# Optimization experiments

Measured on AMD Instinct MI355X. Metric: run time of the kernel, lower is better.

## Reference

```python
import jax, jax.numpy as jnp
import numpy as np

N = 50000        # nodes
E = 800000       # edges (avg degree 16)
G = 64           # graphs in batch
F_IN = 9
OUT = 10


def setup_inputs() -> dict:
    key = jax.random.key(0)
    ks = jax.random.split(key, 20)
    def w(k, fi, fo):
        return jax.random.normal(k, (fi, fo), dtype=jnp.float32) * (1.0 / np.sqrt(fi))
    inp = {
        "x": jax.random.normal(ks[0], (N, F_IN), dtype=jnp.float32),
        "edge_index": jax.random.randint(ks[1], (2, E), 0, N, dtype=jnp.int64),
        "batch": jnp.sort(jax.random.randint(ks[2], (N,), 0, G, dtype=jnp.int64)),
        # GCNConv weights (PyG: x @ W then normalized scatter-add, + bias)
        "W1": w(ks[3], F_IN, 128), "b1": jnp.zeros((128,), jnp.float32),
        "W2": w(ks[4], 128, 256),  "b2": jnp.zeros((256,), jnp.float32),
        "W3": w(ks[5], 256, 256),  "b3": jnp.zeros((256,), jnp.float32),
        "W4": w(ks[6], 256, 256),  "b4": jnp.zeros((256,), jnp.float32),
        # dense head
        "Wl2": w(ks[7], 256, 128), "bl2": jnp.zeros((128,), jnp.float32),
        "Wl3": w(ks[8], 128, 128), "bl3": jnp.zeros((128,), jnp.float32),
        "Wl":  w(ks[9], 128, OUT), "bl":  jnp.zeros((OUT,), jnp.float32),
    }
    return inp


def reference(x, edge_index, batch, W1, b1, W2, b2, W3, b3, W4, b4,
              Wl2, bl2, Wl3, bl3, Wl, bl):
    # GCNConv with self-loops and symmetric deg^{-1/2} normalization
    loops = jnp.arange(N, dtype=edge_index.dtype)
    src = jnp.concatenate([edge_index[0], loops])   # [E+N]
    dst = jnp.concatenate([edge_index[1], loops])
    deg = jax.ops.segment_sum(jnp.ones_like(src, dtype=x.dtype), dst, num_segments=N)
    dinv = jax.lax.rsqrt(deg)                        # deg >= 1 due to self-loops
    norm = (dinv[src] * dinv[dst])[:, None]          # [E+N, 1]

    def conv(h, W, b):
        msg = (h @ W)[src] * norm                    # gather + normalize
        return jax.ops.segment_sum(msg, dst, num_segments=N) + b

    h = jax.nn.relu(conv(x, W1, b1))
    h = jax.nn.relu(conv(h, W2, b2))
    h = jax.nn.relu(conv(h, W3, b3))
    h = conv(h, W4, b4)                              # no relu before pool
    g = jax.ops.segment_max(h, batch, num_segments=G)  # global_max_pool -> [G, 256]
    g = jax.nn.relu(g @ Wl2 + bl2)
    g = jax.nn.relu(g @ Wl3 + bl3)
    out = g @ Wl + bl                                # [G, OUT]
    return jnp.squeeze(out)
```

## Files before the change

### kernel.cpp

```cpp
#include <hip/hip_runtime.h>
#include <float.h>

#define NN 50000
#define NE 800000
#define NG 64
#define CAP 64
#define EPT 16

typedef __attribute__((ext_vector_type(8))) _Float16 f16x8;
typedef __attribute__((ext_vector_type(4))) float f32x4;
typedef __attribute__((ext_vector_type(4))) _Float16 half4;
typedef unsigned int u32;
typedef unsigned short u16;

__device__ __forceinline__ unsigned f2mono(float f) {
  unsigned b = __float_as_uint(f);
  return (b & 0x80000000u) ? ~b : (b | 0x80000000u);
}
__device__ __forceinline__ float mono2f(unsigned u) {
  unsigned b = (u & 0x80000000u) ? (u & 0x7fffffffu) : ~u;
  return __uint_as_float(b);
}
__device__ __forceinline__ void gl_lds16(const void* g, void* l) {
  __builtin_amdgcn_global_load_lds((const __attribute__((address_space(1))) u32*)g,
                                   (__attribute__((address_space(3))) u32*)l, 16, 0, 0);
}

__global__ __launch_bounds__(256) void k_count(const int* __restrict__ src,
                                               const int* __restrict__ dst,
                                               int* __restrict__ cnt,
                                               u16* __restrict__ col) {
  int s = blockIdx.x & 7;
  int base = (blockIdx.x >> 3) * (256 * EPT) + threadIdx.x;
#pragma unroll
  for (int r = 0; r < EPT; ++r) {
    int e = base + r * 256;
    if (e >= NE) break;
    int d = dst[e];
    if ((d & 7) != s) continue;
    if ((unsigned)d >= NN) continue;
    int sv = src[e];
    if ((unsigned)sv >= NN) continue;
    int pos = atomicAdd(&cnt[d], 1);
    if (pos < CAP) col[d * CAP + pos] = (u16)sv;
  }
}

__global__ void k_dinv(const int* __restrict__ cnt, float* __restrict__ dinv,
                       const float* __restrict__ x, float* __restrict__ xs,
                       unsigned* __restrict__ g) {
  int v = blockIdx.x * blockDim.x + threadIdx.x;
  if (v >= NN) return;
  if (v < NG * 256) g[v] = 0u;
  float d = rsqrtf((float)cnt[v] + 1.0f);
  dinv[v] = d;
#pragma unroll
  for (int i = 0; i < 9; ++i) xs[v * 9 + i] = x[v * 9 + i] * d;
}

__device__ __forceinline__ void splitw1(const float* W, _Float16* Wh, _Float16* Wl,
                                        int i, int K, int Nc) {
  int k = i / Nc, n = i - k * Nc;
  float w = W[i];
  _Float16 h = (_Float16)w;
  _Float16 l = (_Float16)(w - (float)h);
  Wh[(size_t)n * K + k] = h;
  Wl[(size_t)n * K + k] = l;
}
__global__ void k_splitw3(const float* __restrict__ W2, const float* __restrict__ W3,
                          const float* __restrict__ W4,
                          _Float16* __restrict__ W2h, _Float16* __restrict__ W2l,
                          _Float16* __restrict__ W3h, _Float16* __restrict__ W3l,
                          _Float16* __restrict__ W4h, _Float16* __restrict__ W4l) {
  int i = blockIdx.x * 256 + threadIdx.x;
  const int n2 = 128 * 256, n3 = 256 * 256;
  if (i < n2) splitw1(W2, W2h, W2l, i, 128, 256);
  else if (i < n2 + n3) splitw1(W3, W3h, W3l, i - n2, 256, 256);
  else if (i < n2 + 2 * n3) splitw1(W4, W4h, W4l, i - n2 - n3, 256, 256);
}

__global__ __launch_bounds__(256) void k_l1(const float* __restrict__ xs,
                                            const float* __restrict__ W,
                                            const float* __restrict__ bias,
                                            const float* __restrict__ dinv,
                                            const int* __restrict__ cnt,
                                            const u16* __restrict__ col,
                                            _Float16* __restrict__ out) {
  __shared__ float sW[9 * 128];
  __shared__ float sb[128];
  __shared__ float sX[16][12];
  int t = threadIdx.x;
  if (t < 128) sb[t] = bias[t];
  for (int i = t; i < 9 * 128; i += 256) sW[i] = W[i];
  int g = t >> 4, l = t & 15;
  int v = blockIdx.x * 16 + g;
  int c = cnt[v]; if (c > CAP) c = CAP;
  const u16* cl = col + (size_t)v * CAP;
  float acc = (l < 9) ? xs[v * 9 + l] : 0.0f;
  int j = 0;
  for (; j + 4 <= c; j += 4) {
    ushort4 u = *(const ushort4*)(cl + j);
    float a0 = (l < 9) ? xs[(int)u.x * 9 + l] : 0.f;
    float a1 = (l < 9) ? xs[(int)u.y * 9 + l] : 0.f;
    float a2 = (l < 9) ? xs[(int)u.z * 9 + l] : 0.f;
    float a3 = (l < 9) ? xs[(int)u.w * 9 + l] : 0.f;
    acc += (a0 + a1) + (a2 + a3);
  }
  for (; j < c; ++j) {
    int u = cl[j];
    if (l < 9) acc += xs[u * 9 + l];
  }
  if (l < 9) sX[g][l] = acc * dinv[v];
  __syncthreads();
  int cc = t & 127;
  int g0 = (t >> 7) * 8;
#pragma unroll
  for (int rr = 0; rr < 8; ++rr) {
    int gi = g0 + rr;
    int r = blockIdx.x * 16 + gi;
    float a = sb[cc];
#pragma unroll
    for (int i = 0; i < 9; ++i) a += sX[gi][i] * sW[i * 128 + cc];
    out[(size_t)r * 128 + cc] = (_Float16)(fmaxf(a, 0.0f) * dinv[r]);
  }
}

__global__ __launch_bounds__(256) void k_aggs(const half4* __restrict__ h,
                                              half4* __restrict__ out,
                                              const int* __restrict__ cnt,
                                              const u16* __restrict__ col,
                                              const float* __restrict__ dinv,
                                              int rowU, int slog) {
  int bid = blockIdx.x;
  int s = bid & ((1 << slog) - 1);
  int chunk = bid >> slog;
  int g = threadIdx.x >> 4;
  int l = threadIdx.x & 15;
  int v = chunk * 16 + g;
  if (v >= NN) return;
  int so = s * 16 + l;
  int c = cnt[v]; if (c > CAP) c = CAP;
  const u16* cl = col + (size_t)v * CAP;
  half4 sv = h[(size_t)v * rowU + so];
  float ax = (float)sv.x, ay = (float)sv.y, az = (float)sv.z, aw = (float)sv.w;
  int j = 0;
  for (; j + 4 <= c; j += 4) {
    ushort4 u = *(const ushort4*)(cl + j);
    half4 t0 = h[(size_t)u.x * rowU + so];
    half4 t1 = h[(size_t)u.y * rowU + so];
    half4 t2 = h[(size_t)u.z * rowU + so];
    half4 t3 = h[(size_t)u.w * rowU + so];
    ax += ((float)t0.x + (float)t1.x) + ((float)t2.x + (float)t3.x);
    ay += ((float)t0.y + (float)t1.y) + ((float)t2.y + (float)t3.y);
    az += ((float)t0.z + (float)t1.z) + ((float)t2.z + (float)t3.z);
    aw += ((float)t0.w + (float)t1.w) + ((float)t2.w + (float)t3.w);
  }
  for (; j < c; ++j) {
    half4 tv = h[(size_t)cl[j] * rowU + so];
    ax += (float)tv.x; ay += (float)tv.y; az += (float)tv.z; aw += (float)tv.w;
  }
  float d = dinv[v];
  half4 o;
  o.x = (_Float16)(ax * d); o.y = (_Float16)(ay * d);
  o.z = (_Float16)(az * d); o.w = (_Float16)(aw * d);
  out[(size_t)v * rowU + so] = o;
}

__global__ __launch_bounds__(256) void k_mm(const _Float16* __restrict__ A,
                                            const _Float16* __restrict__ Bh,
                                            const _Float16* __restrict__ Bl,
                                            const float* __restrict__ bias,
                                            _Float16* __restrict__ C,
                                            const float* __restrict__ dinv,
                                            const int* __restrict__ batch,
                                            unsigned* __restrict__ gpool,
                                            int M, int K, int Nc, int mode) {
  __shared__ __align__(16) _Float16 Alds[128 * 64];
  __shared__ __align__(16) _Float16 Bhl[128 * 64];
  __shared__ __align__(16) _Float16 Bll[128 * 64];
  int bid = blockIdx.x;
  int rblk = (bid >> 4) * 8 + (bid & 7);
  int cblk = (bid >> 3) & 1;
  if (rblk * 128 >= M) return;
  int rowBase = rblk * 128;
  int colBase = cblk * 128;
  int t = threadIdx.x;
  int wave = t >> 6, lane = t & 63;
  int wm = wave & 1, wn = wave >> 1;
  int lm = lane & 15;
  int q  = lane >> 4;

  int srl = wave * 32 + (lane >> 3);
  int sj  = lane & 7;
  int ssw = lane >> 3;
  int gseg = sj ^ ssw;

  f32x4 acc[4][4];
#pragma unroll
  for (int i = 0; i < 4; ++i)
#pragma unroll
    for (int j = 0; j < 4; ++j) acc[i][j] = (f32x4){0.f, 0.f, 0.f, 0.f};

  int nit = K >> 6;
  for (int it = 0; it < nit; ++it) {
    __syncthreads();
#pragma unroll
    for (int c = 0; c < 4; ++c) {
      int rl = srl + c * 8;
      int ga = rowBase + rl; if (ga > M - 1) ga = M - 1;
      int gb = colBase + rl;
      unsigned off = (unsigned)it * 64 + gseg * 8;
      int ldst = (wave * 32 + c * 8) * 64 + lane * 8;
      gl_lds16(A  + (size_t)ga * K + off, Alds + ldst);
      gl_lds16(Bh + (size_t)gb * K + off, Bhl + ldst);
      gl_lds16(Bl + (size_t)gb * K + off, Bll + ldst);
    }
    __syncthreads();

#pragma unroll
    for (int s2 = 0; s2 < 2; ++s2) {
      int slotq = ((s2 << 2) | q);
      f16x8 vbh[4], vbl[4];
#pragma unroll
      for (int ni = 0; ni < 4; ++ni) {
        int rB = wn * 64 + ni * 16 + lm;
        int slot = slotq ^ (lm & 7);
        vbh[ni] = *(const f16x8*)(Bhl + rB * 64 + slot * 8);
        vbl[ni] = *(const f16x8*)(Bll + rB * 64 + slot * 8);
      }
#pragma unroll
      for (int mi = 0; mi < 4; ++mi) {
        int rA = wm * 64 + mi * 16 + lm;
        int slot = slotq ^ (lm & 7);
        f16x8 va = *(const f16x8*)(Alds + rA * 64 + slot * 8);
#pragma unroll
        for (int ni = 0; ni < 4; ++ni) {
          acc[mi][ni] = __builtin_amdgcn_mfma_f32_16x16x32_f16(va, vbh[ni], acc[mi][ni], 0, 0, 0);
          acc[mi][ni] = __builtin_amdgcn_mfma_f32_16x16x32_f16(va, vbl[ni], acc[mi][ni], 0, 0, 0);
        }
      }
    }
  }

  int rowOff = (lane >> 4) * 4;
  if (mode == 2) {
    __syncthreads();
    unsigned* ldsPool = (unsigned*)Alds;
    for (int i = t; i < 4 * 256; i += 256) ldsPool[i] = 0u;
    __syncthreads();
    int b0 = batch[rowBase];
#pragma unroll
    for (int mi = 0; mi < 4; ++mi) {
#pragma unroll
      for (int ni = 0; ni < 4; ++ni) {
        int gc = colBase + wn * 64 + ni * 16 + lm;
        float bsv = bias[gc];
#pragma unroll
        for (int r = 0; r < 4; ++r) {
          int gr = rowBase + wm * 64 + mi * 16 + rowOff + r;
          if (gr < M) {
            float v = acc[mi][ni][r] + bsv;
            int idx = batch[gr] - b0;
            if (idx < 0) idx = 0;
            if (idx > 3) idx = 3;
            atomicMax(&ldsPool[idx * 256 + gc], f2mono(v));
          }
        }
      }
    }
    __syncthreads();
#pragma unroll
    for (int s4 = 0; s4 < 4; ++s4) {
      unsigned mv = ldsPool[s4 * 256 + t];
      int gb = b0 + s4;
      if (mv && gb < NG) atomicMax(&gpool[gb * 256 + t], mv);
    }
  } else {
#pragma unroll
    for (int mi = 0; mi < 4; ++mi) {
#pragma unroll
      for (int ni = 0; ni < 4; ++ni) {
        int gc = colBase + wn * 64 + ni * 16 + lm;
        float bsv = bias[gc];
#pragma unroll
        for (int r = 0; r < 4; ++r) {
          int gr = rowBase + wm * 64 + mi * 16 + rowOff + r;
          if (gr < M) {
            float v = fmaxf(acc[mi][ni][r] + bsv, 0.0f);
            C[(size_t)gr * Nc + gc] = (_Float16)(v * dinv[gr]);
          }
        }
      }
    }
  }
}

__global__ __launch_bounds__(256) void k_head(const unsigned* __restrict__ g,
                                              const float* __restrict__ Wl2, const float* __restrict__ bl2,
                                              const float* __restrict__ Wl3, const float* __restrict__ bl3,
                                              const float* __restrict__ Wl, const float* __restrict__ bl,
                                              float* __restrict__ out) {
  __shared__ float s0[256];
  __shared__ float s1[128];
  __shared__ float s2[128];
  int b = blockIdx.x, t = threadIdx.x;
  s0[t] = mono2f(g[b * 256 + t]);
  __syncthreads();
  if (t < 128) {
    float acc = bl2[t];
    for (int k = 0; k < 256; ++k) acc += s0[k] * Wl2[k * 128 + t];
    s1[t] = fmaxf(acc, 0.0f);
  }
  __syncthreads();
  if (t < 128) {
    float acc = bl3[t];
    for (int k = 0; k < 128; ++k) acc += s1[k] * Wl3[k * 128 + t];
    s2[t] = fmaxf(acc, 0.0f);
  }
  __syncthreads();
  if (t < 10) {
    float acc = bl[t];
    for (int k = 0; k < 128; ++k) acc += s2[k] * Wl[k * 10 + t];
    out[b * 10 + t] = acc;
  }
}

extern "C" void kernel_launch(void* const* d_in, const int* in_sizes, int n_in,
                              void* d_out, int out_size, void* d_ws, size_t ws_size,
                              hipStream_t stream) {
  const float* x   = (const float*)d_in[0];
  const int* eidx  = (const int*)d_in[1];
  const int* batch = (const int*)d_in[2];
  const float* W1 = (const float*)d_in[3];   const float* b1 = (const float*)d_in[4];
  const float* W2 = (const float*)d_in[5];   const float* b2 = (const float*)d_in[6];
  const float* W3 = (const float*)d_in[7];   const float* b3 = (const float*)d_in[8];
  const float* W4 = (const float*)d_in[9];   const float* b4 = (const float*)d_in[10];
  const float* Wl2 = (const float*)d_in[11]; const float* bl2 = (const float*)d_in[12];
  const float* Wl3 = (const float*)d_in[13]; const float* bl3 = (const float*)d_in[14];
  const float* Wl  = (const float*)d_in[15]; const float* bl  = (const float*)d_in[16];
  float* out = (float*)d_out;

  _Float16* bufA = (_Float16*)d_ws;
  _Float16* bufB = bufA + (size_t)NN * 256;
  int* cnt  = (int*)(bufB + (size_t)NN * 256);
  float* dinv = (float*)(cnt + NN);
  u16* col  = (u16*)(dinv + NN);
  unsigned* g = (unsigned*)(col + (size_t)NN * CAP);
  _Float16* W2h = (_Float16*)(g + NG * 256);
  _Float16* W2l = W2h + 256 * 128;
  _Float16* W3h = W2l + 256 * 128;
  _Float16* W3l = W3h + 256 * 256;
  _Float16* W4h = W3l + 256 * 256;
  _Float16* W4l = W4h + 256 * 256;
  float* xs = (float*)bufB;

  const int* src = eidx;
  const int* dst = eidx + NE;

  hipMemsetAsync(cnt, 0, NN * sizeof(int), stream);

  const int cntGrid = 8 * ((NE + 256 * EPT - 1) / (256 * EPT));
  k_count<<<cntGrid, 256, 0, stream>>>(src, dst, cnt, col);
  k_dinv<<<(NN + 255) / 256, 256, 0, stream>>>(cnt, dinv, x, xs, g);

  k_splitw3<<<(128 * 256 + 2 * 256 * 256 + 255) / 256, 256, 0, stream>>>(
      W2, W3, W4, W2h, W2l, W3h, W3l, W4h, W4l);

  const int nchunk = (NN + 15) / 16;
  const int mmGrid = 784;

  k_l1<<<nchunk, 256, 0, stream>>>(xs, W1, b1, dinv, cnt, col, bufA);

  k_aggs<<<nchunk * 2, 256, 0, stream>>>((const half4*)bufA, (half4*)bufB, cnt, col, dinv, 32, 1);
  k_mm<<<mmGrid, 256, 0, stream>>>(bufB, W2h, W2l, b2, bufA, dinv, batch, g, NN, 128, 256, 1);

  k_aggs<<<nchunk * 4, 256, 0, stream>>>((const half4*)bufA, (half4*)bufB, cnt, col, dinv, 64, 2);
  k_mm<<<mmGrid, 256, 0, stream>>>(bufB, W3h, W3l, b3, bufA, dinv, batch, g, NN, 256, 256, 1);

  k_aggs<<<nchunk * 4, 256, 0, stream>>>((const half4*)bufA, (half4*)bufB, cnt, col, dinv, 64, 2);
  k_mm<<<mmGrid, 256, 0, stream>>>(bufB, W4h, W4l, b4, bufA, dinv, batch, g, NN, 256, 256, 2);

  k_head<<<NG, 256, 0, stream>>>(g, Wl2, bl2, Wl3, bl3, Wl, bl, out);
}
```

Before: 404.3 us.

## Prefetch next K-tile into registers while computing current tile in GEMM

Replaces the direct global-to-LDS async loads with register-staged loads: the next K-slice of A, Bh and Bl is fetched into registers before the MFMA loop for the current slice, then written to LDS after a barrier. Per-row global offsets are hoisted out of the loop. The aim is to overlap global memory latency with MFMA compute instead of stalling on each tile load. It costs extra VGPRs (12 f16x8 vectors), which may reduce occupancy, and routes data through registers rather than using the global-to-LDS path.

```diff
diff --git a/kernel.cpp b/kernel.cpp
--- a/kernel.cpp
+++ b/kernel.cpp
@@ -195,6 +195,17 @@
   int ssw = lane >> 3;
   int gseg = sj ^ ssw;
 
+  size_t gaRow[4], gbRow[4];
+  int ldst[4];
+#pragma unroll
+  for (int c = 0; c < 4; ++c) {
+    int rl = srl + c * 8;
+    int ga = rowBase + rl; if (ga > M - 1) ga = M - 1;
+    gaRow[c] = (size_t)ga * K + gseg * 8;
+    gbRow[c] = (size_t)(colBase + rl) * K + gseg * 8;
+    ldst[c] = (wave * 32 + c * 8) * 64 + lane * 8;
+  }
+
   f32x4 acc[4][4];
 #pragma unroll
   for (int i = 0; i < 4; ++i)
@@ -202,36 +213,46 @@
     for (int j = 0; j < 4; ++j) acc[i][j] = (f32x4){0.f, 0.f, 0.f, 0.f};
 
   int nit = K >> 6;
+  f16x8 ra[4], rh[4], rb[4];
+#pragma unroll
+  for (int c = 0; c < 4; ++c) {
+    ra[c] = *(const f16x8*)(A  + gaRow[c]);
+    rh[c] = *(const f16x8*)(Bh + gbRow[c]);
+    rb[c] = *(const f16x8*)(Bl + gbRow[c]);
+  }
+#pragma unroll
+  for (int c = 0; c < 4; ++c) {
+    *(f16x8*)(Alds + ldst[c]) = ra[c];
+    *(f16x8*)(Bhl  + ldst[c]) = rh[c];
+    *(f16x8*)(Bll  + ldst[c]) = rb[c];
+  }
+  __syncthreads();
+
   for (int it = 0; it < nit; ++it) {
-    __syncthreads();
-#pragma unroll
-    for (int c = 0; c < 4; ++c) {
-      int rl = srl + c * 8;
-      int ga = rowBase + rl; if (ga > M - 1) ga = M - 1;
-      int gb = colBase + rl;
-      unsigned off = (unsigned)it * 64 + gseg * 8;
-      int ldst = (wave * 32 + c * 8) * 64 + lane * 8;
-      gl_lds16(A  + (size_t)ga * K + off, Alds + ldst);
-      gl_lds16(Bh + (size_t)gb * K + off, Bhl + ldst);
-      gl_lds16(Bl + (size_t)gb * K + off, Bll + ldst);
-    }
-    __syncthreads();
+    if (it + 1 < nit) {
+      size_t off = (size_t)(it + 1) * 64;
+#pragma unroll
+      for (int c = 0; c < 4; ++c) {
+        ra[c] = *(const f16x8*)(A  + gaRow[c] + off);
+        rh[c] = *(const f16x8*)(Bh + gbRow[c] + off);
+        rb[c] = *(const f16x8*)(Bl + gbRow[c] + off);
+      }
+    }
 
 #pragma unroll
     for (int s2 = 0; s2 < 2; ++s2) {
       int slotq = ((s2 << 2) | q);
+      int slot = slotq ^ (lm & 7);
       f16x8 vbh[4], vbl[4];
 #pragma unroll
       for (int ni = 0; ni < 4; ++ni) {
         int rB = wn * 64 + ni * 16 + lm;
-        int slot = slotq ^ (lm & 7);
         vbh[ni] = *(const f16x8*)(Bhl + rB * 64 + slot * 8);
         vbl[ni] = *(const f16x8*)(Bll + rB * 64 + slot * 8);
       }
 #pragma unroll
       for (int mi = 0; mi < 4; ++mi) {
         int rA = wm * 64 + mi * 16 + lm;
-        int slot = slotq ^ (lm & 7);
         f16x8 va = *(const f16x8*)(Alds + rA * 64 + slot * 8);
 #pragma unroll
         for (int ni = 0; ni < 4; ++ni) {
@@ -239,6 +260,16 @@
           acc[mi][ni] = __builtin_amdgcn_mfma_f32_16x16x32_f16(va, vbl[ni], acc[mi][ni], 0, 0, 0);
         }
       }
+    }
+    __syncthreads();
+    if (it + 1 < nit) {
+#pragma unroll
+      for (int c = 0; c < 4; ++c) {
+        *(f16x8*)(Alds + ldst[c]) = ra[c];
+        *(f16x8*)(Bhl  + ldst[c]) = rh[c];
+        *(f16x8*)(Bll  + ldst[c]) = rb[c];
+      }
+      __syncthreads();
     }
   }
 
```

Measured after the change: 414.5 us. +2.5%, slower.

## Pad neighbor lists with a zero sentinel row and vectorize edge loads

Applied to the files above, without the earlier changes.

Unused slots in each node's neighbor list are padded with an index pointing to an extra zeroed row appended to the feature buffers. This lets the aggregation loop step through neighbors eight at a time with a single vector index load and no scalar tail. The edge-counting kernel now reads destination indices as int4 vectors, four per thread per round. The cost is extra zero-row gathers for degrees that are not multiples of eight, plus padding writes in k_dinv.

```diff
diff --git a/kernel.cpp b/kernel.cpp
--- a/kernel.cpp
+++ b/kernel.cpp
@@ -5,13 +5,14 @@
 #define NE 800000
 #define NG 64
 #define CAP 64
-#define EPT 16
 
 typedef __attribute__((ext_vector_type(8))) _Float16 f16x8;
 typedef __attribute__((ext_vector_type(4))) float f32x4;
 typedef __attribute__((ext_vector_type(4))) _Float16 half4;
+typedef __attribute__((ext_vector_type(8))) unsigned short u16x8;
 typedef unsigned int u32;
 typedef unsigned short u16;
+typedef unsigned long long u64;
 
 __device__ __forceinline__ unsigned f2mono(float f) {
   unsigned b = __float_as_uint(f);
@@ -31,31 +32,51 @@
                                                int* __restrict__ cnt,
                                                u16* __restrict__ col) {
   int s = blockIdx.x & 7;
-  int base = (blockIdx.x >> 3) * (256 * EPT) + threadIdx.x;
-#pragma unroll
-  for (int r = 0; r < EPT; ++r) {
-    int e = base + r * 256;
-    if (e >= NE) break;
-    int d = dst[e];
-    if ((d & 7) != s) continue;
-    if ((unsigned)d >= NN) continue;
-    int sv = src[e];
-    if ((unsigned)sv >= NN) continue;
-    int pos = atomicAdd(&cnt[d], 1);
-    if (pos < CAP) col[d * CAP + pos] = (u16)sv;
+  int base = (blockIdx.x >> 3) * 4096;
+  const int4* dst4 = (const int4*)dst;
+  int4 q[4];
+  int ei[4];
+  bool ok[4];
+#pragma unroll
+  for (int r = 0; r < 4; ++r) {
+    ei[r] = base + (r * 256 + (int)threadIdx.x) * 4;
+    ok[r] = ei[r] < NE;
+    if (ok[r]) q[r] = dst4[ei[r] >> 2];
+  }
+#pragma unroll
+  for (int r = 0; r < 4; ++r) {
+    if (!ok[r]) continue;
+    int dd0 = q[r].x, dd1 = q[r].y, dd2 = q[r].z, dd3 = q[r].w;
+#pragma unroll
+    for (int k = 0; k < 4; ++k) {
+      int d = (k == 0) ? dd0 : (k == 1) ? dd1 : (k == 2) ? dd2 : dd3;
+      if ((d & 7) != s) continue;
+      if ((unsigned)d >= NN) continue;
+      int sv = src[ei[r] + k];
+      if ((unsigned)sv >= NN) continue;
+      int pos = atomicAdd(&cnt[d], 1);
+      if (pos < CAP) col[d * CAP + pos] = (u16)sv;
+    }
   }
 }
 
 __global__ void k_dinv(const int* __restrict__ cnt, float* __restrict__ dinv,
                        const float* __restrict__ x, float* __restrict__ xs,
-                       unsigned* __restrict__ g) {
+                       unsigned* __restrict__ g, u16* __restrict__ col,
+                       _Float16* __restrict__ bufA) {
   int v = blockIdx.x * blockDim.x + threadIdx.x;
   if (v >= NN) return;
   if (v < NG * 256) g[v] = 0u;
-  float d = rsqrtf((float)cnt[v] + 1.0f);
+  if (v < 32) ((u64*)(bufA + (size_t)NN * 128))[v] = 0ULL;
+  if (v < 64) ((u64*)(bufA + (size_t)NN * 256))[v] = 0ULL;
+  int cc = cnt[v];
+  float d = rsqrtf((float)cc + 1.0f);
   dinv[v] = d;
 #pragma unroll
   for (int i = 0; i < 9; ++i) xs[v * 9 + i] = x[v * 9 + i] * d;
+  int c = cc > CAP ? CAP : cc;
+  u16* cr = col + (size_t)v * CAP;
+  for (int i = c; i < CAP; ++i) cr[i] = (u16)NN;
 }
 
 __device__ __forceinline__ void splitw1(const float* W, _Float16* Wh, _Float16* Wl,
@@ -141,23 +162,27 @@
   int so = s * 16 + l;
   int c = cnt[v]; if (c > CAP) c = CAP;
   const u16* cl = col + (size_t)v * CAP;
-  half4 sv = h[(size_t)v * rowU + so];
+  const half4* hb = h + so;
+  half4 sv = hb[(size_t)v * rowU];
   float ax = (float)sv.x, ay = (float)sv.y, az = (float)sv.z, aw = (float)sv.w;
-  int j = 0;
-  for (; j + 4 <= c; j += 4) {
-    ushort4 u = *(const ushort4*)(cl + j);
-    half4 t0 = h[(size_t)u.x * rowU + so];
-    half4 t1 = h[(size_t)u.y * rowU + so];
-    half4 t2 = h[(size_t)u.z * rowU + so];
-    half4 t3 = h[(size_t)u.w * rowU + so];
-    ax += ((float)t0.x + (float)t1.x) + ((float)t2.x + (float)t3.x);
-    ay += ((float)t0.y + (float)t1.y) + ((float)t2.y + (float)t3.y);
-    az += ((float)t0.z + (float)t1.z) + ((float)t2.z + (float)t3.z);
-    aw += ((float)t0.w + (float)t1.w) + ((float)t2.w + (float)t3.w);
-  }
-  for (; j < c; ++j) {
-    half4 tv = h[(size_t)cl[j] * rowU + so];
-    ax += (float)tv.x; ay += (float)tv.y; az += (float)tv.z; aw += (float)tv.w;
+  for (int j = 0; j < c; j += 8) {
+    u16x8 u = *(const u16x8*)(cl + j);
+    half4 t0 = hb[(size_t)u[0] * rowU];
+    half4 t1 = hb[(size_t)u[1] * rowU];
+    half4 t2 = hb[(size_t)u[2] * rowU];
+    half4 t3 = hb[(size_t)u[3] * rowU];
+    half4 t4 = hb[(size_t)u[4] * rowU];
+    half4 t5 = hb[(size_t)u[5] * rowU];
+    half4 t6 = hb[(size_t)u[6] * rowU];
+    half4 t7 = hb[(size_t)u[7] * rowU];
+    ax += (((float)t0.x + (float)t1.x) + ((float)t2.x + (float)t3.x)) +
+          (((float)t4.x + (float)t5.x) + ((float)t6.x + (float)t7.x));
+    ay += (((float)t0.y + (float)t1.y) + ((float)t2.y + (float)t3.y)) +
+          (((float)t4.y + (float)t5.y) + ((float)t6.y + (float)t7.y));
+    az += (((float)t0.z + (float)t1.z) + ((float)t2.z + (float)t3.z)) +
+          (((float)t4.z + (float)t5.z) + ((float)t6.z + (float)t7.z));
+    aw += (((float)t0.w + (float)t1.w) + ((float)t2.w + (float)t3.w)) +
+          (((float)t4.w + (float)t5.w) + ((float)t6.w + (float)t7.w));
   }
   float d = dinv[v];
   half4 o;
@@ -341,8 +366,8 @@
   float* out = (float*)d_out;
 
   _Float16* bufA = (_Float16*)d_ws;
-  _Float16* bufB = bufA + (size_t)NN * 256;
-  int* cnt  = (int*)(bufB + (size_t)NN * 256);
+  _Float16* bufB = bufA + (size_t)(NN + 1) * 256;
+  int* cnt  = (int*)(bufB + (size_t)(NN + 1) * 256);
   float* dinv = (float*)(cnt + NN);
   u16* col  = (u16*)(dinv + NN);
   unsigned* g = (unsigned*)(col + (size_t)NN * CAP);
@@ -359,9 +384,9 @@
 
   hipMemsetAsync(cnt, 0, NN * sizeof(int), stream);
 
-  const int cntGrid = 8 * ((NE + 256 * EPT - 1) / (256 * EPT));
+  const int cntGrid = 8 * ((NE + 4095) / 4096);
   k_count<<<cntGrid, 256, 0, stream>>>(src, dst, cnt, col);
-  k_dinv<<<(NN + 255) / 256, 256, 0, stream>>>(cnt, dinv, x, xs, g);
+  k_dinv<<<(NN + 255) / 256, 256, 0, stream>>>(cnt, dinv, x, xs, g, col, bufA);
 
   k_splitw3<<<(128 * 256 + 2 * 256 * 256 + 255) / 256, 256, 0, stream>>>(
       W2, W3, W4, W2h, W2l, W3h, W3l, W4h, W4l);
```

Measured after the change: 388.8 us, median of 2. 3.8% less time.
